# Kernel optimization log

Hardware: AMD Instinct MI355X
Metric: run time of the kernel (lower is better)

Reference implementation:

```python
import jax, jax.numpy as jnp
import numpy as np

IDIM = 128   # idim == odim (fc1 input dim must match shift-slice width idim_q)
HDIM = 1024
CDIM = 256
IGNORE_OUT = 10000.0


def setup_inputs() -> dict:
    key = jax.random.key(0)
    ks = jax.random.split(key, 4)
    B, T = 4, 512
    x = jax.random.normal(ks[0], (B, T, IDIM), dtype=jnp.float32)
    y = jax.random.normal(ks[1], (B, T, IDIM), dtype=jnp.float32)
    # xavier-ish init for the two linears (bias zeroed, as in initialize())
    w1 = jax.random.normal(ks[2], (HDIM, IDIM), dtype=jnp.float32) / np.sqrt(IDIM).astype(np.float32)
    b1 = jnp.zeros((HDIM,), jnp.float32)
    w2 = jax.random.normal(ks[3], (IDIM, HDIM), dtype=jnp.float32) / np.sqrt(HDIM).astype(np.float32)
    b2 = jnpts = jnp.zeros((IDIM,), jnp.float32)
    return {"x": x, "y": y, "w1": w1, "b1": b1, "w2": w2, "b2": b2}


def _shift_stack(key_seq, idim):
    """Vectorized _pad_for_shift: (B,T,idim) -> (B,T,2*idim-1,idim) shifted slices."""
    pad = idim - 1
    kp = jnp.pad(key_seq, ((0, 0), (0, 0), (pad, pad)))  # (B,T,3*idim-2)
    idx = jnp.arange(2 * idim - 1)[:, None] + jnp.arange(idim)[None, :]  # (S, idim)
    return kp[..., idx]  # (B,T,S,idim)


def _forward(x, y, w1, b1, w2, b2):
    idim = IDIM
    n_iter = HDIM // CDIM
    seq_mask = (y == IGNORE_OUT)                      # (B,T,odim)
    denom = jnp.sum(~seq_mask).astype(x.dtype)
    y_res, x_res = y, x
    losses = []
    for i in range(n_iter):
        # --- argaug (scale=False): sliding cosine cross-correlation + argmax ---
        kpt = _shift_stack(x_res, idim)               # (B,T,S,idim), S=2*idim-1
        num = jnp.einsum('btd,btsd->bts', y_res, kpt)
        den = jnp.linalg.norm(y_res, axis=-1)[..., None] * jnp.linalg.norm(kpt, axis=-1)
        sim = jnp.where(den == 0, 0.0, num / jnp.where(den == 0, 1.0, den))  # NaN(0/0) -> 0
        idx = jnp.argmax(sim, axis=-1)                # (B,T), first max like torch.max
        x_aug = jnp.take_along_axis(kpt, idx[..., None, None], axis=2)[..., 0, :]  # (B,T,idim)
        # --- attention (detached) ---
        attn = jax.lax.stop_gradient(jax.nn.softmax(x_aug * y_res, axis=-1))
        x_attn = x_aug * attn
        # --- _reverse_pad_for_shift: un-shift x_attn by 2*idim-2 - idx ---
        pad = idim - 1
        xap = jnp.pad(x_attn, ((0, 0), (0, 0), (pad, pad)))
        ridx = (2 * idim - 2 - idx)[..., None] + jnp.arange(idim)  # (B,T,idim)
        x_ele = jnp.take_along_axis(xap, ridx, axis=-1)
        # --- channel-masked two-layer MLP ---
        h = x_attn @ w1.T + b1                        # (B,T,hdim)
        m = jnp.zeros((HDIM,), x.dtype).at[i * CDIM:(i + 1) * CDIM].set(1.0)
        y_ele = (h * m) @ w2.T + b2                   # (B,T,odim)
        # --- masked MSE (sum of masked squared errors / #unmasked) ---
        sq = jnp.where(seq_mask, 0.0, (y_ele - y_res) ** 2)
        losses.append(jnp.sum(sq) / denom)
        y_res = y_res - y_ele
        x_res = x_res - x_ele
    return jnp.mean(jnp.stack(losses))


def reference(x, y, w1, b1, w2, b2):
    return _forward(x, y, w1, b1, w2, b2)
```

## Files before the change

kernel.cpp:

```cpp
#include <hip/hip_runtime.h>
#include <math.h>

#define NROWS   2048
#define NITER   4
#define IGNORE_OUT 10000.0f


__device__ __forceinline__ float waveSum(float v){
  #pragma unroll
  for (int o = 32; o; o >>= 1) v += __shfl_down(v, o, 64);
  return v;
}

__device__ __forceinline__ float blkSum(float v, float* red){
  v = waveSum(v);
  int lane = threadIdx.x & 63, wid = threadIdx.x >> 6;
  __syncthreads();
  if (lane == 0) red[wid] = v;
  __syncthreads();
  return red[0] + red[1] + red[2] + red[3];
}

__device__ __forceinline__ float blkMax(float v, float* red){
  #pragma unroll
  for (int o = 32; o; o >>= 1) v = fmaxf(v, __shfl_down(v, o, 64));
  int lane = threadIdx.x & 63, wid = threadIdx.x >> 6;
  __syncthreads();
  if (lane == 0) red[wid] = v;
  __syncthreads();
  return fmaxf(fmaxf(red[0], red[1]), fmaxf(red[2], red[3]));
}

__device__ __forceinline__ int blkArgmaxFirst(float v, int idx, float* redv, int* redi){
  #pragma unroll
  for (int o = 32; o; o >>= 1){
    float ov = __shfl_down(v,   o, 64);
    int   oi = __shfl_down(idx, o, 64);
    if (ov > v || (ov == v && oi < idx)) { v = ov; idx = oi; }
  }
  int lane = threadIdx.x & 63, wid = threadIdx.x >> 6;
  __syncthreads();
  if (lane == 0){ redv[wid] = v; redi[wid] = idx; }
  __syncthreads();
  float bv = redv[0]; int bi = redi[0];
  #pragma unroll
  for (int w = 1; w < 4; ++w){
    float ov = redv[w]; int oi = redi[w];
    if (ov > bv || (ov == bv && oi < bi)) { bv = ov; bi = oi; }
  }
  return bi;
}

__global__ void buildM(const float* __restrict__ w1, const float* __restrict__ w2,
                       float* __restrict__ Mt){
  int blk = blockIdx.x;
  int i = blk >> 7, o = blk & 127;
  int d = threadIdx.x;
  const float* w1p = w1 + (i * 256) * 128 + d;
  const float* w2p = w2 + o * 1024 + i * 256;
  float acc = 0.f;
  #pragma unroll 8
  for (int c = 0; c < 256; ++c)
    acc = fmaf(w1p[c * 128], w2p[c], acc);
  Mt[(i * 128 + d) * 128 + o] = acc;
}

__global__ void biasK(const float* __restrict__ b1, const float* __restrict__ b2,
                      const float* __restrict__ w2, float* __restrict__ biasT){
  int i = blockIdx.x;
  int o = threadIdx.x;
  const float* w2p = w2 + o * 1024 + i * 256;
  const float* b1p = b1 + i * 256;
  float a = b2[o];
  #pragma unroll 8
  for (int c = 0; c < 256; ++c) a = fmaf(b1p[c], w2p[c], a);
  biasT[i * 128 + o] = a;
}

__global__ __launch_bounds__(256)
void mainK(const float* __restrict__ x, const float* __restrict__ y,
           const float* __restrict__ Mt, const float* __restrict__ biasT,
           float* __restrict__ acc){
  __shared__ float xr[128];
  __shared__ float yr[128];
  __shared__ float xatt[128];
  __shared__ float part[256];
  __shared__ float redf[4];
  __shared__ int   redi[4];

  const int tid = threadIdx.x;
  const long base = (long)blockIdx.x * 128;

  float lossAcc = 0.f;
  float cnt = 0.f;
  bool  maskv = false;
  if (tid < 128){
    xr[tid] = x[base + tid];
    float yv = y[base + tid];
    yr[tid] = yv;
    maskv = (yv == IGNORE_OUT);
    cnt = maskv ? 0.f : 1.f;
  }
  __syncthreads();

  for (int i = 0; i < NITER; ++i){
    float sy = (tid < 128) ? yr[tid] * yr[tid] : 0.f;
    float ny2 = blkSum(sy, redf);
    float nY = sqrtf(ny2);

    float num = 0.f, nx2 = 0.f;
    {
      int s  = tid;
      int d0 = 127 - s; if (d0 < 0)   d0 = 0;
      int d1 = 254 - s; if (d1 > 127) d1 = 127;
      int jb = s - 127;
      for (int d = d0; d <= d1; ++d){
        float w = xr[jb + d];
        num = fmaf(yr[d], w, num);
        nx2 = fmaf(w, w, nx2);
      }
    }
    float den = nY * sqrtf(nx2);
    float sim = (den == 0.f) ? 0.f : num / den;
    if (tid >= 255) sim = -INFINITY;
    int sstar = blkArgmaxFirst(sim, tid, redf, redi);

    float xa = 0.f, z = -INFINITY;
    if (tid < 128){
      int j = sstar + tid - 127;
      xa = ((unsigned)j < 128u) ? xr[j] : 0.f;
      z  = xa * yr[tid];
    }
    float mz = blkMax(z, redf);
    float e  = (tid < 128) ? expf(z - mz) : 0.f;
    float se = blkSum(e, redf);
    if (tid < 128) xatt[tid] = xa * (e / se);
    __syncthreads();

    if (tid < 128){
      int j2 = tid + 127 - sstar;
      float xe = ((unsigned)j2 < 128u) ? xatt[j2] : 0.f;
      xr[tid] -= xe;
    }

    {
      int o = tid & 127, half = tid >> 7;
      const float* Mi = Mt + i * 16384 + o;
      int dbeg = half * 64;
      float a2 = 0.f;
      #pragma unroll 8
      for (int d = 0; d < 64; ++d)
        a2 = fmaf(Mi[(dbeg + d) * 128], xatt[dbeg + d], a2);
      part[tid] = a2;
    }
    __syncthreads();
    if (tid < 128){
      float ye   = part[tid] + part[tid + 128] + biasT[i * 128 + tid];
      float diff = ye - yr[tid];
      if (!maskv) lossAcc = fmaf(diff, diff, lossAcc);
      yr[tid] = -diff;
    }
    __syncthreads();
  }

  float tot  = blkSum(lossAcc, redf);
  float totc = blkSum(cnt, redf);
  if (tid == 0){
    atomicAdd(&acc[0], tot);
    atomicAdd(&acc[1], totc);
  }
}

__global__ void finalize(const float* __restrict__ acc, float* __restrict__ out){
  if (threadIdx.x == 0 && blockIdx.x == 0)
    out[0] = acc[0] / ((float)NITER * acc[1]);
}

extern "C" void kernel_launch(void* const* d_in, const int* in_sizes, int n_in,
                              void* d_out, int out_size, void* d_ws, size_t ws_size,
                              hipStream_t stream){
  const float* x  = (const float*)d_in[0];
  const float* y  = (const float*)d_in[1];
  const float* w1 = (const float*)d_in[2];
  const float* b1 = (const float*)d_in[3];
  const float* w2 = (const float*)d_in[4];
  const float* b2 = (const float*)d_in[5];
  float* out = (float*)d_out;

  float* accp  = (float*)d_ws;
  float* Mt    = (float*)((char*)d_ws + 256);
  float* biasT = (float*)((char*)d_ws + 256 + 4 * 128 * 128 * sizeof(float));

  hipMemsetAsync(d_ws, 0, 2 * sizeof(float), stream);
  buildM<<<512, 128, 0, stream>>>(w1, w2, Mt);
  biasK<<<4, 128, 0, stream>>>(b1, b2, w2, biasT);
  mainK<<<NROWS, 256, 0, stream>>>(x, y, Mt, biasT, accp);
  finalize<<<1, 64, 0, stream>>>(accp, out);
}
```

Measured before the change: 185.9 us.

## Balance cross-correlation work via prefix-sum norms and merge prep kernels

The sliding cross-correlation is restructured. Each thread now handles two shifts (s and s+128), computing full and partial dot products against a duplicated y buffer with float4 loads of x. The shifted-slice norms come from a prefix sum of x squared instead of per-shift loops, which removes the triangular load imbalance across threads. The weight-folding, bias and accumulator-zeroing kernels plus the memset are merged into one prep launch to cut launch overhead. The cost is more shared-memory passes and barriers per iteration, and prefix-sum norms may differ slightly from the direct sums in floating point.

```diff
diff --git a/kernel.cpp b/kernel.cpp
--- a/kernel.cpp
+++ b/kernel.cpp
@@ -6,14 +6,9 @@
 #define IGNORE_OUT 10000.0f
 
 
-__device__ __forceinline__ float waveSum(float v){
+__device__ __forceinline__ float blkSum(float v, float* red){
   #pragma unroll
   for (int o = 32; o; o >>= 1) v += __shfl_down(v, o, 64);
-  return v;
-}
-
-__device__ __forceinline__ float blkSum(float v, float* red){
-  v = waveSum(v);
   int lane = threadIdx.x & 63, wid = threadIdx.x >> 6;
   __syncthreads();
   if (lane == 0) red[wid] = v;
@@ -51,121 +46,184 @@
   return bi;
 }
 
-__global__ void buildM(const float* __restrict__ w1, const float* __restrict__ w2,
-                       float* __restrict__ Mt){
-  int blk = blockIdx.x;
-  int i = blk >> 7, o = blk & 127;
-  int d = threadIdx.x;
-  const float* w1p = w1 + (i * 256) * 128 + d;
-  const float* w2p = w2 + o * 1024 + i * 256;
-  float acc = 0.f;
-  #pragma unroll 8
-  for (int c = 0; c < 256; ++c)
-    acc = fmaf(w1p[c * 128], w2p[c], acc);
-  Mt[(i * 128 + d) * 128 + o] = acc;
-}
-
-__global__ void biasK(const float* __restrict__ b1, const float* __restrict__ b2,
-                      const float* __restrict__ w2, float* __restrict__ biasT){
-  int i = blockIdx.x;
-  int o = threadIdx.x;
-  const float* w2p = w2 + o * 1024 + i * 256;
-  const float* b1p = b1 + i * 256;
-  float a = b2[o];
-  #pragma unroll 8
-  for (int c = 0; c < 256; ++c) a = fmaf(b1p[c], w2p[c], a);
-  biasT[i * 128 + o] = a;
-}
-
 __global__ __launch_bounds__(256)
+void prepK(const float* __restrict__ w1, const float* __restrict__ b1,
+           const float* __restrict__ w2, const float* __restrict__ b2,
+           float* __restrict__ Mt, float* __restrict__ biasT, float* __restrict__ acc){
+  __shared__ float part[256];
+  const int blk = blockIdx.x;
+  const int u = threadIdx.x;
+  if (blk < 512){
+    int i = blk >> 7, o = blk & 127;
+    int d = u & 127, ch = u >> 7;
+    const float* w1p = w1 + (i * 256 + ch * 128) * 128 + d;
+    const float* w2p = w2 + o * 1024 + i * 256 + ch * 128;
+    float a = 0.f;
+    #pragma unroll 16
+    for (int c = 0; c < 128; ++c) a = fmaf(w1p[c * 128], w2p[c], a);
+    part[u] = a;
+    __syncthreads();
+    if (u < 128) Mt[(i * 128 + u) * 128 + o] = part[u] + part[u + 128];
+  } else if (blk < 516){
+    int i = blk - 512;
+    if (u < 128){
+      const float* w2p = w2 + u * 1024 + i * 256;
+      const float* b1p = b1 + i * 256;
+      float a = b2[u];
+      #pragma unroll 8
+      for (int c = 0; c < 256; ++c) a = fmaf(b1p[c], w2p[c], a);
+      biasT[i * 128 + u] = a;
+    }
+  } else {
+    if (u < 2) acc[u] = 0.f;
+  }
+}
+
+__global__ __launch_bounds__(256, 8)
 void mainK(const float* __restrict__ x, const float* __restrict__ y,
            const float* __restrict__ Mt, const float* __restrict__ biasT,
            float* __restrict__ acc){
-  __shared__ float xr[128];
-  __shared__ float yr[128];
+  __shared__ alignas(16) float xr[128];
+  __shared__ float yd[384];
   __shared__ float xatt[128];
-  __shared__ float part[256];
+  __shared__ float pn1[256];
+  __shared__ float pnt[256];
+  __shared__ float pref[128];
+  __shared__ float wtot[2];
   __shared__ float redf[4];
   __shared__ int   redi[4];
 
-  const int tid = threadIdx.x;
+  const int u    = threadIdx.x;
+  const int lane = u & 63;
+  const int wid  = u >> 6;
+  const int t    = u & 127;
+  const int h    = u >> 7;
+  const int jb   = h * 64;
   const long base = (long)blockIdx.x * 128;
 
-  float lossAcc = 0.f;
-  float cnt = 0.f;
+  float lossAcc = 0.f, cnt = 0.f;
   bool  maskv = false;
-  if (tid < 128){
-    xr[tid] = x[base + tid];
-    float yv = y[base + tid];
-    yr[tid] = yv;
+  float xv = 0.f, yv = 0.f;
+  if (u < 128){
+    xv = x[base + u];
+    yv = y[base + u];
+    xr[u] = xv;
     maskv = (yv == IGNORE_OUT);
     cnt = maskv ? 0.f : 1.f;
   }
   __syncthreads();
 
   for (int i = 0; i < NITER; ++i){
-    float sy = (tid < 128) ? yr[tid] * yr[tid] : 0.f;
-    float ny2 = blkSum(sy, redf);
-    float nY = sqrtf(ny2);
-
-    float num = 0.f, nx2 = 0.f;
+    float v = (u < 128) ? xv * xv : 0.f;
+    #pragma unroll
+    for (int o2 = 1; o2 < 64; o2 <<= 1){
+      float tv = __shfl_up(v, o2, 64);
+      if (lane >= o2) v += tv;
+    }
+    __syncthreads();
+    if (u < 128 && lane == 63) wtot[u >> 6] = v;
+    if (u < 128){ yd[128 + u] = yv; yd[256 + u] = yv; }
+    __syncthreads();
+    float total = wtot[0] + wtot[1];
+    if (u >= 64 && u < 128) v += wtot[0];
+    if (u < 128) pref[u] = v;
+    float ny2 = blkSum((u < 128) ? yv * yv : 0.f, redf);
+
     {
-      int s  = tid;
-      int d0 = 127 - s; if (d0 < 0)   d0 = 0;
-      int d1 = 254 - s; if (d1 > 127) d1 = 127;
-      int jb = s - 127;
-      for (int d = d0; d <= d1; ++d){
-        float w = xr[jb + d];
-        num = fmaf(yr[d], w, num);
-        nx2 = fmaf(w, w, nx2);
+      const float* ydp = yd + (255 - t);
+      float n1 = 0.f, nt = 0.f;
+      if (wid == 1){
+        #pragma unroll 4
+        for (int j = 0; j < 64; j += 4){
+          float4 x4 = *(const float4*)&xr[j];
+          n1 = fmaf(ydp[j + 0], x4.x, n1);
+          n1 = fmaf(ydp[j + 1], x4.y, n1);
+          n1 = fmaf(ydp[j + 2], x4.z, n1);
+          n1 = fmaf(ydp[j + 3], x4.w, n1);
+        }
+        nt = n1;
+      } else if (wid == 2){
+        #pragma unroll 4
+        for (int j = 64; j < 128; j += 4){
+          float4 x4 = *(const float4*)&xr[j];
+          nt = fmaf(ydp[j + 0], x4.x, nt);
+          nt = fmaf(ydp[j + 1], x4.y, nt);
+          nt = fmaf(ydp[j + 2], x4.z, nt);
+          nt = fmaf(ydp[j + 3], x4.w, nt);
+        }
+      } else {
+        #pragma unroll 4
+        for (int j = jb; j < jb + 64; j += 4){
+          float4 x4 = *(const float4*)&xr[j];
+          float p;
+          p = ydp[j + 0] * x4.x; nt += p; n1 += (j + 0 <= t) ? p : 0.f;
+          p = ydp[j + 1] * x4.y; nt += p; n1 += (j + 1 <= t) ? p : 0.f;
+          p = ydp[j + 2] * x4.z; nt += p; n1 += (j + 2 <= t) ? p : 0.f;
+          p = ydp[j + 3] * x4.w; nt += p; n1 += (j + 3 <= t) ? p : 0.f;
+        }
       }
-    }
-    float den = nY * sqrtf(nx2);
-    float sim = (den == 0.f) ? 0.f : num / den;
-    if (tid >= 255) sim = -INFINITY;
-    int sstar = blkArgmaxFirst(sim, tid, redf, redi);
+      pn1[u] = n1; pnt[u] = nt;
+    }
+    __syncthreads();
+
+    float simv = -INFINITY; int sidx = 1000 + u;
+    if (u < 128){
+      float a1 = pn1[u] + pn1[u + 128];
+      float at = pnt[u] + pnt[u + 128];
+      float a2 = at - a1;
+      float nY  = sqrtf(ny2);
+      float nx1 = pref[u];
+      float nx2 = fmaxf(total - pref[u], 0.f);
+      float den1 = nY * sqrtf(nx1);
+      float den2 = nY * sqrtf(nx2);
+      float s1 = (den1 == 0.f) ? 0.f : a1 / den1;
+      float s2 = (den2 == 0.f) ? 0.f : a2 / den2;
+      if (u == 127) s2 = -INFINITY;
+      if (s1 >= s2){ simv = s1; sidx = u; } else { simv = s2; sidx = u + 128; }
+    }
+    int sstar = blkArgmaxFirst(simv, sidx, redf, redi);
 
     float xa = 0.f, z = -INFINITY;
-    if (tid < 128){
-      int j = sstar + tid - 127;
+    if (u < 128){
+      int j = sstar + u - 127;
       xa = ((unsigned)j < 128u) ? xr[j] : 0.f;
-      z  = xa * yr[tid];
+      z  = xa * yv;
     }
     float mz = blkMax(z, redf);
-    float e  = (tid < 128) ? expf(z - mz) : 0.f;
+    float e  = (u < 128) ? expf(z - mz) : 0.f;
     float se = blkSum(e, redf);
-    if (tid < 128) xatt[tid] = xa * (e / se);
-    __syncthreads();
-
-    if (tid < 128){
-      int j2 = tid + 127 - sstar;
+    if (u < 128) xatt[u] = xa * (e / se);
+    __syncthreads();
+
+    if (u < 128){
+      int j2 = u + 127 - sstar;
       float xe = ((unsigned)j2 < 128u) ? xatt[j2] : 0.f;
-      xr[tid] -= xe;
+      xv -= xe;
+      xr[u] = xv;
     }
 
     {
-      int o = tid & 127, half = tid >> 7;
-      const float* Mi = Mt + i * 16384 + o;
-      int dbeg = half * 64;
+      const float* Mi = Mt + i * 16384 + t + jb * 128;
       float a2 = 0.f;
-      #pragma unroll 8
+      #pragma unroll 16
       for (int d = 0; d < 64; ++d)
-        a2 = fmaf(Mi[(dbeg + d) * 128], xatt[dbeg + d], a2);
-      part[tid] = a2;
-    }
-    __syncthreads();
-    if (tid < 128){
-      float ye   = part[tid] + part[tid + 128] + biasT[i * 128 + tid];
-      float diff = ye - yr[tid];
+        a2 = fmaf(Mi[d * 128], xatt[jb + d], a2);
+      pn1[u] = a2;
+    }
+    __syncthreads();
+
+    if (u < 128){
+      float ye   = pn1[u] + pn1[u + 128] + biasT[i * 128 + u];
+      float diff = ye - yv;
       if (!maskv) lossAcc = fmaf(diff, diff, lossAcc);
-      yr[tid] = -diff;
+      yv = -diff;
     }
     __syncthreads();
   }
 
   float tot  = blkSum(lossAcc, redf);
   float totc = blkSum(cnt, redf);
-  if (tid == 0){
+  if (u == 0){
     atomicAdd(&acc[0], tot);
     atomicAdd(&acc[1], totc);
   }
@@ -191,9 +249,7 @@
   float* Mt    = (float*)((char*)d_ws + 256);
   float* biasT = (float*)((char*)d_ws + 256 + 4 * 128 * 128 * sizeof(float));
 
-  hipMemsetAsync(d_ws, 0, 2 * sizeof(float), stream);
-  buildM<<<512, 128, 0, stream>>>(w1, w2, Mt);
-  biasK<<<4, 128, 0, stream>>>(b1, b2, w2, biasT);
+  prepK<<<517, 256, 0, stream>>>(w1, b1, w2, b2, Mt, biasT, accp);
   mainK<<<NROWS, 256, 0, stream>>>(x, y, Mt, biasT, accp);
   finalize<<<1, 64, 0, stream>>>(accp, out);
 }
```

Result: slower. 212.0 us (+14.0%).
